# Kernel tuning notes

Measured on AMD Instinct MI355X. Metric: run time of the kernel, lower is better.

## Reference

```python
import jax, jax.numpy as jnp
import numpy as np

B, S, C, H, EPS = 8, 1024, 768, 12, 1e-6
D = C // H            # head dim 64
F_HID = int(C * 4.0)  # 3072


def _layer_norm(x, w, b):
    mu = jnp.mean(x, axis=-1, keepdims=True)
    var = jnp.mean(jnp.square(x - mu), axis=-1, keepdims=True)
    return (x - mu) * jax.lax.rsqrt(var + EPS) * w + b


def setup_inputs() -> dict:
    key = jax.random.key(0)
    ks = jax.random.split(key, 16)
    sc_c = 1.0 / np.sqrt(C)
    sc_f = 1.0 / np.sqrt(F_HID)
    return {
        "hidden_states": jax.random.normal(ks[0], (B, S, C), jnp.float32),
        "ln1_w": jnp.ones((C,), jnp.float32),
        "ln1_b": jnp.zeros((C,), jnp.float32),
        # weights stored [in, out] (transpose of torch Linear layout; same math)
        "q_w": jax.random.normal(ks[1], (C, C), jnp.float32) * sc_c,
        "q_b": jnp.zeros((C,), jnp.float32),
        "k_w": jax.random.normal(ks[2], (C, C), jnp.float32) * sc_c,
        "k_b": jnp.zeros((C,), jnp.float32),
        "v_w": jax.random.normal(ks[3], (C, C), jnp.float32) * sc_c,
        "v_b": jnp.zeros((C,), jnp.float32),
        "o_w": jax.random.normal(ks[4], (C, C), jnp.float32) * sc_c,
        "o_b": jnp.zeros((C,), jnp.float32),
        "lam1": jnp.ones((C,), jnp.float32),
        "ln2_w": jnp.ones((C,), jnp.float32),
        "ln2_b": jnp.zeros((C,), jnp.float32),
        "fc1_w": jax.random.normal(ks[5], (C, F_HID), jnp.float32) * sc_c,
        "fc1_b": jnp.zeros((F_HID,), jnp.float32),
        "fc2_w": jax.random.normal(ks[6], (F_HID, C), jnp.float32) * sc_f,
        "fc2_b": jnp.zeros((C,), jnp.float32),
    }


def reference(hidden_states, ln1_w, ln1_b, q_w, q_b, k_w, k_b, v_w, v_b,
              o_w, o_b, lam1, ln2_w, ln2_b, fc1_w, fc1_b, fc2_w, fc2_b):
    shortcut = hidden_states
    x = _layer_norm(hidden_states, ln1_w, ln1_b)
    # QKV projections, split heads: [B,S,C] -> [B,H,S,D]
    def heads(t):
        return t.reshape(B, S, H, D).transpose(0, 2, 1, 3)
    q = heads(x @ q_w + q_b)
    k = heads(x @ k_w + k_b)
    v = heads(x @ v_w + v_b)
    scores = jnp.einsum("bhsd,bhtd->bhst", q, k) / np.sqrt(D)
    probs = jax.nn.softmax(scores, axis=-1)  # dropout p=0 -> identity
    ctx = jnp.einsum("bhst,bhtd->bhsd", probs, v)
    ctx = ctx.transpose(0, 2, 1, 3).reshape(B, S, C)
    attn_out = ctx @ o_w + o_b
    hidden = attn_out * lam1 + shortcut
    y = _layer_norm(hidden, ln2_w, ln2_b)
    y = jax.nn.gelu(y @ fc1_w + fc1_b, approximate=False)
    y = y @ fc2_w + fc2_b
    return y * lam2_mul(lam1) + hidden if False else (y * jnp.ones_like(lam1) * lam1 * 0 + y) * 0 + y * lam1 * 0 + (y * _LAM2 + hidden)


# NOTE: layer_scale2 has its own parameter; expose it cleanly instead of the hack above.
_LAM2 = None

def lam2_mul(x):
    return x

# Clean final definitions (override the above):

def setup_inputs() -> dict:  # noqa: F811
    key = jax.random.key(0)
    ks = jax.random.split(key, 16)
    sc_c = 1.0 / np.sqrt(C)
    sc_f = 1.0 / np.sqrt(F_HID)
    return {
        "hidden_states": jax.random.normal(ks[0], (B, S, C), jnp.float32),
        "ln1_w": jnp.ones((C,), jnp.float32),
        "ln1_b": jnp.zeros((C,), jnp.float32),
        "q_w": jax.random.normal(ks[1], (C, C), jnp.float32) * sc_c,
        "q_b": jnp.zeros((C,), jnp.float32),
        "k_w": jax.random.normal(ks[2], (C, C), jnp.float32) * sc_c,
        "k_b": jnp.zeros((C,), jnp.float32),
        "v_w": jax.random.normal(ks[3], (C, C), jnp.float32) * sc_c,
        "v_b": jnp.zeros((C,), jnp.float32),
        "o_w": jax.random.normal(ks[4], (C, C), jnp.float32) * sc_c,
        "o_b": jnp.zeros((C,), jnp.float32),
        "lam1": jnp.ones((C,), jnp.float32),
        "ln2_w": jnp.ones((C,), jnp.float32),
        "ln2_b": jnp.zeros((C,), jnp.float32),
        "fc1_w": jax.random.normal(ks[5], (C, F_HID), jnp.float32) * sc_c,
        "fc1_b": jnp.zeros((F_HID,), jnp.float32),
        "fc2_w": jax.random.normal(ks[6], (F_HID, C), jnp.float32) * sc_f,
        "fc2_b": jnp.zeros((C,), jnp.float32),
        "lam2": jnp.ones((C,), jnp.float32),
    }


def reference(hidden_states, ln1_w, ln1_b, q_w, q_b, k_w, k_b, v_w, v_b,  # noqa: F811
              o_w, o_b, lam1, ln2_w, ln2_b, fc1_w, fc1_b, fc2_w, fc2_b, lam2):
    shortcut = hidden_states
    x = _layer_norm(hidden_states, ln1_w, ln1_b)
    def heads(t):
        return t.reshape(B, S, H, D).transpose(0, 2, 1, 3)  # [B,H,S,D]
    q = heads(x @ q_w + q_b)
    k = heads(x @ k_w + k_b)
    v = heads(x @ v_w + v_b)
    scores = jnp.einsum("bhsd,bhtd->bhst", q, k) / np.sqrt(D)
    probs = jax.nn.softmax(scores, axis=-1)  # attn dropout p=0 (eval)
    ctx = jnp.einsum("bhst,bhtd->bhsd", probs, v)
    ctx = ctx.transpose(0, 2, 1, 3).reshape(B, S, C)
    attn_out = ctx @ o_w + o_b            # SelfOutput dense (dropout p=0)
    hidden = attn_out * lam1 + shortcut   # layer_scale1 + residual
    y = _layer_norm(hidden, ln2_w, ln2_b)
    y = jax.nn.gelu(y @ fc1_w + fc1_b, approximate=False)  # nn.GELU exact
    y = y @ fc2_w + fc2_b
    return y * lam2 + hidden              # layer_scale2 + residual
```

## Files before the change

### kernel.cpp

```cpp
#include <hip/hip_runtime.h>
#include <hip/hip_bf16.h>
#include <stdint.h>
#include <stddef.h>

using bf16x8 = __attribute__((ext_vector_type(8))) short;
using f32x4  = __attribute__((ext_vector_type(4))) float;
using f32x16 = __attribute__((ext_vector_type(16))) float;

#define DEV static __device__ __forceinline__

DEV unsigned short f2bf(float f) {
  union { float f; uint32_t u; } x; x.f = f;
  uint32_t u = x.u;
  u += 0x7fffu + ((u >> 16) & 1u);
  return (unsigned short)(u >> 16);
}

DEV uint32_t pkbf(float a, float b) {
  __hip_bfloat162 t = __float22bfloat162_rn(float2{a, b});
  union { __hip_bfloat162 h; uint32_t u; } c; c.h = t; return c.u;
}

DEV void gld_lds16(const void* g, void* lds) {
  __builtin_amdgcn_global_load_lds(
      (__attribute__((address_space(1))) void*)(uintptr_t)g,
      (__attribute__((address_space(3))) void*)(uintptr_t)lds, 16, 0, 0);
}

__global__ void transpose_w(const float* __restrict__ in, unsigned short* __restrict__ out,
                            int K, int N) {
  __shared__ float tile[64][65];
  int n0 = blockIdx.x * 64, k0 = blockIdx.y * 64;
  int tx = threadIdx.x & 15, ty = threadIdx.x >> 4;
#pragma unroll
  for (int j = 0; j < 4; ++j) {
    int r = ty + j * 16;
    float4 v = *(const float4*)(in + (size_t)(k0 + r) * N + n0 + tx * 4);
    tile[r][tx * 4 + 0] = v.x; tile[r][tx * 4 + 1] = v.y;
    tile[r][tx * 4 + 2] = v.z; tile[r][tx * 4 + 3] = v.w;
  }
  __syncthreads();
#pragma unroll
  for (int j = 0; j < 4; ++j) {
    int n = ty + j * 16;
    ushort4 o;
    o.x = f2bf(tile[tx * 4 + 0][n]);
    o.y = f2bf(tile[tx * 4 + 1][n]);
    o.z = f2bf(tile[tx * 4 + 2][n]);
    o.w = f2bf(tile[tx * 4 + 3][n]);
    *(ushort4*)(out + (size_t)(n0 + n) * K + k0 + tx * 4) = o;
  }
}

__global__ void pack_bias(const float* __restrict__ q, const float* __restrict__ k,
                          const float* __restrict__ v, float* __restrict__ out) {
  int i = blockIdx.x * 256 + threadIdx.x;
  const float* s = (i < 768) ? q : ((i < 1536) ? k : v);
  int r = i; if (r >= 1536) r -= 1536; else if (r >= 768) r -= 768;
  out[i] = s[r];
}

__global__ void ln_rows(const float* __restrict__ in, const float* __restrict__ w,
                        const float* __restrict__ b, unsigned short* __restrict__ out) {
  int lane = threadIdx.x & 63;
  int row = blockIdx.x * 4 + (threadIdx.x >> 6);
  const float* p = in + (size_t)row * 768;
  float4 v[3];
  float s = 0.f, s2 = 0.f;
#pragma unroll
  for (int j = 0; j < 3; ++j) {
    v[j] = *(const float4*)(p + j * 256 + lane * 4);
    s  += v[j].x + v[j].y + v[j].z + v[j].w;
    s2 += v[j].x * v[j].x + v[j].y * v[j].y + v[j].z * v[j].z + v[j].w * v[j].w;
  }
#pragma unroll
  for (int o = 32; o >= 1; o >>= 1) { s += __shfl_xor(s, o); s2 += __shfl_xor(s2, o); }
  float mu = s * (1.f / 768.f);
  float var = s2 * (1.f / 768.f) - mu * mu;
  float rs = rsqrtf(var + 1e-6f);
#pragma unroll
  for (int j = 0; j < 3; ++j) {
    int c = j * 256 + lane * 4;
    float4 wv = *(const float4*)(w + c);
    float4 bv = *(const float4*)(b + c);
    ushort4 o4;
    o4.x = f2bf((v[j].x - mu) * rs * wv.x + bv.x);
    o4.y = f2bf((v[j].y - mu) * rs * wv.y + bv.y);
    o4.z = f2bf((v[j].z - mu) * rs * wv.z + bv.z);
    o4.w = f2bf((v[j].w - mu) * rs * wv.w + bv.w);
    *(ushort4*)(out + (size_t)row * 768 + c) = o4;
  }
}

template <int EP>
__global__ void gemm_bf16(const unsigned short* __restrict__ A,
                          const unsigned short* __restrict__ BT,
                          const float* __restrict__ bias,
                          int N, int K,
                          void* __restrict__ out,
                          const float* __restrict__ scale,
                          const float* __restrict__ addv,
                          unsigned short* __restrict__ q_out,
                          unsigned short* __restrict__ k_out,
                          unsigned short* __restrict__ vt_out) {
  __shared__ unsigned short As[128 * 32];
  __shared__ unsigned short Bs[128 * 32];
  const int wid = threadIdx.x >> 6, lane = threadIdx.x & 63;
  const int bm = blockIdx.y * 128, bn = blockIdx.x * 128;
  const int wr = wid >> 1, wc = wid & 1;
  f32x4 acc[4][4] = {};

  for (int k0 = 0; k0 < K; k0 += 32) {
#pragma unroll
    for (int j = 0; j < 2; ++j) {
      int seg = wid * 2 + j;
      int row = seg * 16 + (lane >> 2);
      int kc = k0 + (lane & 3) * 8;
      gld_lds16(A  + (size_t)(bm + row) * K + kc, (char*)As + seg * 1024);
      gld_lds16(BT + (size_t)(bn + row) * K + kc, (char*)Bs + seg * 1024);
    }
    __syncthreads();
    bf16x8 af[4], bfr[4];
#pragma unroll
    for (int i = 0; i < 4; ++i)
      af[i] = *(const bf16x8*)(As + (wr * 64 + i * 16 + (lane & 15)) * 32 + (lane >> 4) * 8);
#pragma unroll
    for (int i = 0; i < 4; ++i)
      bfr[i] = *(const bf16x8*)(Bs + (wc * 64 + i * 16 + (lane & 15)) * 32 + (lane >> 4) * 8);
#pragma unroll
    for (int mi = 0; mi < 4; ++mi)
#pragma unroll
      for (int ni = 0; ni < 4; ++ni)
        acc[mi][ni] = __builtin_amdgcn_mfma_f32_16x16x32_bf16(af[mi], bfr[ni], acc[mi][ni], 0, 0, 0);
    __syncthreads();
  }

#pragma unroll
  for (int mi = 0; mi < 4; ++mi) {
#pragma unroll
    for (int ni = 0; ni < 4; ++ni) {
      int col = bn + wc * 64 + ni * 16 + (lane & 15);
      float bcol = bias[col];
#pragma unroll
      for (int r = 0; r < 4; ++r) {
        int row = bm + wr * 64 + mi * 16 + (lane >> 4) * 4 + r;
        float v = acc[mi][ni][r] + bcol;
        if (EP == 0) {
          int b = row >> 10, s = row & 1023;
          int piece = col / 768;
          int rc = col - piece * 768;
          int h = rc >> 6, d = rc & 63;
          unsigned short bvv = f2bf(v);
          if (piece == 0)      q_out [((size_t)(b * 12 + h) * 1024 + s) * 64 + d] = bvv;
          else if (piece == 1) k_out [((size_t)(b * 12 + h) * 1024 + s) * 64 + d] = bvv;
          else                 vt_out[((size_t)(b * 12 + h) * 64 + d) * 1024 + s] = bvv;
        } else if (EP == 1) {
          ((float*)out)[(size_t)row * 768 + col] = v * scale[col] + addv[(size_t)row * 768 + col];
        } else if (EP == 2) {
          float g = 0.5f * v * (1.f + erff(v * 0.70710678118654752f));
          ((unsigned short*)out)[(size_t)row * (size_t)N + col] = f2bf(g);
        } else {
          ((float*)out)[(size_t)row * 768 + col] = v * scale[col] + addv[(size_t)row * 768 + col];
        }
      }
    }
  }
}

__global__ __launch_bounds__(256) void attn_fwd(const unsigned short* __restrict__ qb,
                         const unsigned short* __restrict__ kb,
                         const unsigned short* __restrict__ vtb,
                         unsigned short* __restrict__ ctx) {
  __shared__ unsigned short Ks[2][64 * 64];
  __shared__ unsigned short VTs[2][64 * 64];
  __shared__ float alphaW[4][32];
  const int tid = threadIdx.x;
  const int wid = tid >> 6, lane = tid & 63;
  const int l31 = lane & 31;
  const bool hi = lane >= 32;
  const int hi8 = hi ? 8 : 0, hi16 = hi ? 16 : 0;
  const int sw0 = (l31 & 7) << 4;
  const int wg = (blockIdx.x & 7) * 96 + (blockIdx.x >> 3);
  const int bh = wg >> 3, qt = wg & 7;
  const int b = bh / 12, h = bh % 12;
  const unsigned short* qh  = qb  + (size_t)bh * 1024 * 64;
  const unsigned short* kh  = kb  + (size_t)bh * 1024 * 64;
  const unsigned short* vth = vtb + (size_t)bh * 64 * 1024;

  const int qrow = qt * 128 + wid * 32 + l31;
  bf16x8 qf[4];
#pragma unroll
  for (int kf = 0; kf < 4; ++kf)
    qf[kf] = *(const bf16x8*)(qh + (size_t)qrow * 64 + kf * 16 + hi8);

  bf16x8 ones;
#pragma unroll
  for (int i = 0; i < 8; ++i) ones[i] = (short)0x3F80;

  f32x16 o0 = {}, o1 = {}, l_acc = {};
  float mcol = -1e30f;
  const float sc = 0.125f * 1.44269504088896f;

  const int r1 = tid >> 3;
  const int sl = tid & 7;
  const int cb = (sl * 16) ^ ((r1 & 7) << 4);

  {
    uint4 k0v = *(const uint4*)(kh + (size_t)r1 * 64 + sl * 8);
    uint4 k1v = *(const uint4*)(kh + (size_t)(r1 + 32) * 64 + sl * 8);
    uint4 v0v = *(const uint4*)(vth + (size_t)r1 * 1024 + sl * 8);
    uint4 v1v = *(const uint4*)(vth + (size_t)(r1 + 32) * 1024 + sl * 8);
    *(uint4*)((char*)Ks[0]  + r1 * 128 + cb) = k0v;
    *(uint4*)((char*)Ks[0]  + (r1 + 32) * 128 + cb) = k1v;
    *(uint4*)((char*)VTs[0] + r1 * 128 + cb) = v0v;
    *(uint4*)((char*)VTs[0] + (r1 + 32) * 128 + cb) = v1v;
  }

  uint4 kA, kB, vA, vB;
  for (int t = 0; t < 16; ++t) {
    if (t < 15) {
      const int s1 = (t + 1) * 64;
      kA = *(const uint4*)(kh + (size_t)(s1 + r1) * 64 + sl * 8);
      kB = *(const uint4*)(kh + (size_t)(s1 + r1 + 32) * 64 + sl * 8);
      vA = *(const uint4*)(vth + (size_t)r1 * 1024 + s1 + sl * 8);
      vB = *(const uint4*)(vth + (size_t)(r1 + 32) * 1024 + s1 + sl * 8);
    }
    asm volatile("s_waitcnt lgkmcnt(0)" ::: "memory");
    __builtin_amdgcn_s_barrier();
    const char* KsB  = (const char*)Ks[t & 1];
    const char* VTsB = (const char*)VTs[t & 1];

    f32x16 s0 = {}, s1v = {};
#pragma unroll
    for (int kf = 0; kf < 4; ++kf) {
      bf16x8 k0 = *(const bf16x8*)(KsB + l31 * 128 + ((kf * 32 + hi16) ^ sw0));
      bf16x8 k1 = *(const bf16x8*)(KsB + (l31 + 32) * 128 + ((kf * 32 + hi16) ^ sw0));
      s0  = __builtin_amdgcn_mfma_f32_32x32x16_bf16(k0, qf[kf], s0, 0, 0, 0);
      s1v = __builtin_amdgcn_mfma_f32_32x32x16_bf16(k1, qf[kf], s1v, 0, 0, 0);
    }

    float mt = s0[0];
#pragma unroll
    for (int i = 1; i < 16; ++i) mt = fmaxf(mt, s0[i]);
#pragma unroll
    for (int i = 0; i < 16; ++i) mt = fmaxf(mt, s1v[i]);
    mt *= sc;
    mt = fmaxf(mt, __shfl_xor(mt, 32));

    if (__ballot(mt > mcol + 8.f)) {
      float mnew = fmaxf(mcol, mt);
      float a = exp2f(mcol - mnew);
      if (lane < 32) alphaW[wid][lane] = a;
      mcol = mnew;
      asm volatile("s_waitcnt lgkmcnt(0)" ::: "memory");
      __builtin_amdgcn_sched_barrier(0);
#pragma unroll
      for (int r = 0; r < 16; ++r) {
        float av = alphaW[wid][(r & 3) + ((r >> 2) << 3) + (hi ? 4 : 0)];
        o0[r] *= av; o1[r] *= av; l_acc[r] *= av;
      }
    }

    float p0[16], p1[16];
#pragma unroll
    for (int i = 0; i < 16; ++i) p0[i] = exp2f(s0[i] * sc - mcol);
#pragma unroll
    for (int i = 0; i < 16; ++i) p1[i] = exp2f(s1v[i] * sc - mcol);
    uint32_t W[16], X[16];
#pragma unroll
    for (int i = 0; i < 8; ++i) {
      W[i]     = pkbf(p0[2 * i], p0[2 * i + 1]);
      W[8 + i] = pkbf(p1[2 * i], p1[2 * i + 1]);
    }
#pragma unroll
    for (int i = 0; i < 16; ++i) X[i] = (uint32_t)__shfl_xor((int)W[i], 32);
    bf16x8 pa[4];
    {
      union U4 { uint32_t u[4]; bf16x8 v; } f;
      f.u[0] = hi ? X[2] : W[0];  f.u[1] = hi ? X[3] : W[1];
      f.u[2] = hi ? W[2] : X[0];  f.u[3] = hi ? W[3] : X[1];   pa[0] = f.v;
      f.u[0] = hi ? X[6] : W[4];  f.u[1] = hi ? X[7] : W[5];
      f.u[2] = hi ? W[6] : X[4];  f.u[3] = hi ? W[7] : X[5];   pa[1] = f.v;
      f.u[0] = hi ? X[10] : W[8]; f.u[1] = hi ? X[11] : W[9];
      f.u[2] = hi ? W[10] : X[8]; f.u[3] = hi ? W[11] : X[9];  pa[2] = f.v;
      f.u[0] = hi ? X[14] : W[12]; f.u[1] = hi ? X[15] : W[13];
      f.u[2] = hi ? W[14] : X[12]; f.u[3] = hi ? W[15] : X[13]; pa[3] = f.v;
    }

#pragma unroll
    for (int f = 0; f < 4; ++f) {
      l_acc = __builtin_amdgcn_mfma_f32_32x32x16_bf16(pa[f], ones, l_acc, 0, 0, 0);
      bf16x8 v0 = *(const bf16x8*)(VTsB + l31 * 128 + ((f * 32 + hi16) ^ sw0));
      bf16x8 v1 = *(const bf16x8*)(VTsB + (l31 + 32) * 128 + ((f * 32 + hi16) ^ sw0));
      o0 = __builtin_amdgcn_mfma_f32_32x32x16_bf16(pa[f], v0, o0, 0, 0, 0);
      o1 = __builtin_amdgcn_mfma_f32_32x32x16_bf16(pa[f], v1, o1, 0, 0, 0);
    }

    if (t < 15) {
      asm volatile("s_waitcnt vmcnt(0)" ::: "memory");
      __builtin_amdgcn_sched_barrier(0);
      char* Kn = (char*)Ks[(t + 1) & 1];
      char* Vn = (char*)VTs[(t + 1) & 1];
      *(uint4*)(Kn + r1 * 128 + cb) = kA;
      *(uint4*)(Kn + (r1 + 32) * 128 + cb) = kB;
      *(uint4*)(Vn + r1 * 128 + cb) = vA;
      *(uint4*)(Vn + (r1 + 32) * 128 + cb) = vB;
    }
  }

#pragma unroll
  for (int r = 0; r < 16; ++r) {
    int rq = (r & 3) + ((r >> 2) << 3) + (hi ? 4 : 0);
    int srow = qt * 128 + wid * 32 + rq;
    float inv = 1.f / l_acc[r];
    size_t base = ((size_t)(b * 1024 + srow)) * 768 + h * 64;
    ctx[base + l31]      = f2bf(o0[r] * inv);
    ctx[base + 32 + l31] = f2bf(o1[r] * inv);
  }
}

extern "C" void kernel_launch(void* const* d_in, const int* in_sizes, int n_in,
                              void* d_out, int out_size, void* d_ws, size_t ws_size,
                              hipStream_t stream) {
  const float* hs    = (const float*)d_in[0];
  const float* ln1_w = (const float*)d_in[1];
  const float* ln1_b = (const float*)d_in[2];
  const float* q_w   = (const float*)d_in[3];
  const float* q_b   = (const float*)d_in[4];
  const float* k_w   = (const float*)d_in[5];
  const float* k_b   = (const float*)d_in[6];
  const float* v_w   = (const float*)d_in[7];
  const float* v_b   = (const float*)d_in[8];
  const float* o_w   = (const float*)d_in[9];
  const float* o_b   = (const float*)d_in[10];
  const float* lam1  = (const float*)d_in[11];
  const float* ln2_w = (const float*)d_in[12];
  const float* ln2_b = (const float*)d_in[13];
  const float* fc1_w = (const float*)d_in[14];
  const float* fc1_b = (const float*)d_in[15];
  const float* fc2_w = (const float*)d_in[16];
  const float* fc2_b = (const float*)d_in[17];
  const float* lam2  = (const float*)d_in[18];

  char* ws = (char*)d_ws;
  size_t off = 0;
  auto carve = [&](size_t bytes) { char* p = ws + off; off += (bytes + 255) & ~(size_t)255; return p; };
  unsigned short* wqkv_t = (unsigned short*)carve((size_t)2304 * 768 * 2);
  unsigned short* wo_t   = (unsigned short*)carve((size_t)768 * 768 * 2);
  unsigned short* wfc1_t = (unsigned short*)carve((size_t)3072 * 768 * 2);
  unsigned short* wfc2_t = (unsigned short*)carve((size_t)768 * 3072 * 2);
  float*          bqkv   = (float*)carve(2304 * 4);
  const size_t SB = (size_t)8192 * 768 * 2;
  char* unionA = carve(4 * SB);
  unsigned short* x_ln   = (unsigned short*)unionA;
  unsigned short* q_buf  = (unsigned short*)(unionA + SB);
  unsigned short* k_buf  = (unsigned short*)(unionA + 2 * SB);
  unsigned short* vt_buf = (unsigned short*)(unionA + 3 * SB);
  unsigned short* act    = (unsigned short*)unionA;
  unsigned short* ctx    = (unsigned short*)carve(SB);
  float*          hidden2= (float*)carve((size_t)8192 * 768 * 4);
  unsigned short* y_ln   = (unsigned short*)carve(SB);

  pack_bias<<<dim3(9), dim3(256), 0, stream>>>(q_b, k_b, v_b, bqkv);
  transpose_w<<<dim3(12, 12), dim3(256), 0, stream>>>(q_w, wqkv_t, 768, 768);
  transpose_w<<<dim3(12, 12), dim3(256), 0, stream>>>(k_w, wqkv_t + (size_t)768 * 768, 768, 768);
  transpose_w<<<dim3(12, 12), dim3(256), 0, stream>>>(v_w, wqkv_t + (size_t)2 * 768 * 768, 768, 768);
  transpose_w<<<dim3(12, 12), dim3(256), 0, stream>>>(o_w, wo_t, 768, 768);
  transpose_w<<<dim3(48, 12), dim3(256), 0, stream>>>(fc1_w, wfc1_t, 768, 3072);
  transpose_w<<<dim3(12, 48), dim3(256), 0, stream>>>(fc2_w, wfc2_t, 3072, 768);

  ln_rows<<<dim3(2048), dim3(256), 0, stream>>>(hs, ln1_w, ln1_b, x_ln);
  gemm_bf16<0><<<dim3(18, 64), dim3(256), 0, stream>>>(x_ln, wqkv_t, bqkv, 2304, 768,
      nullptr, nullptr, nullptr, q_buf, k_buf, vt_buf);
  attn_fwd<<<dim3(768), dim3(256), 0, stream>>>(q_buf, k_buf, vt_buf, ctx);
  gemm_bf16<1><<<dim3(6, 64), dim3(256), 0, stream>>>(ctx, wo_t, o_b, 768, 768,
      hidden2, lam1, hs, nullptr, nullptr, nullptr);
  ln_rows<<<dim3(2048), dim3(256), 0, stream>>>(hidden2, ln2_w, ln2_b, y_ln);
  gemm_bf16<2><<<dim3(24, 64), dim3(256), 0, stream>>>(y_ln, wfc1_t, fc1_b, 3072, 768,
      act, nullptr, nullptr, nullptr, nullptr, nullptr);
  gemm_bf16<3><<<dim3(6, 64), dim3(256), 0, stream>>>(act, wfc2_t, fc2_b, 768, 3072,
      d_out, lam2, hidden2, nullptr, nullptr, nullptr);
}
```

Before: 441.1 us.

## Double-buffer GEMM LDS tiles and remap workgroups across XCDs

Double-buffers the A/B shared-memory tiles so the global-to-LDS load for the next K step is issued before the MFMA work on the current tile, leaving one barrier per iteration. It also remaps the workgroup index so consecutive tiles spread over the 8 XCDs, aiming at better L2 locality. The cost is twice the LDS footprint, which can lower occupancy, plus a remap that assumes the tile count divides by 8.

```diff
diff --git a/kernel.cpp b/kernel.cpp
--- a/kernel.cpp
+++ b/kernel.cpp
@@ -103,36 +103,57 @@
                           unsigned short* __restrict__ q_out,
                           unsigned short* __restrict__ k_out,
                           unsigned short* __restrict__ vt_out) {
-  __shared__ unsigned short As[128 * 32];
-  __shared__ unsigned short Bs[128 * 32];
+  __shared__ unsigned short As[2][128 * 32];
+  __shared__ unsigned short Bs[2][128 * 32];
   const int wid = threadIdx.x >> 6, lane = threadIdx.x & 63;
-  const int bm = blockIdx.y * 128, bn = blockIdx.x * 128;
+  const int gx = gridDim.x;
+  const int nwg = gx * gridDim.y;
+  const int bid0 = blockIdx.x + gx * blockIdx.y;
+  const int wg = (bid0 & 7) * (nwg >> 3) + (bid0 >> 3);
+  const int bm = (wg / gx) * 128, bn = (wg % gx) * 128;
   const int wr = wid >> 1, wc = wid & 1;
-  f32x4 acc[4][4] = {};
-
-  for (int k0 = 0; k0 < K; k0 += 32) {
+  const int NT = K >> 5;
+
+  auto stage = [&](int t, int buf) {
+    int k0 = t << 5;
 #pragma unroll
     for (int j = 0; j < 2; ++j) {
       int seg = wid * 2 + j;
       int row = seg * 16 + (lane >> 2);
       int kc = k0 + (lane & 3) * 8;
-      gld_lds16(A  + (size_t)(bm + row) * K + kc, (char*)As + seg * 1024);
-      gld_lds16(BT + (size_t)(bn + row) * K + kc, (char*)Bs + seg * 1024);
-    }
-    __syncthreads();
+      gld_lds16(A  + (size_t)(bm + row) * K + kc, (char*)As[buf] + seg * 1024);
+      gld_lds16(BT + (size_t)(bn + row) * K + kc, (char*)Bs[buf] + seg * 1024);
+    }
+  };
+
+  f32x4 acc[4][4] = {};
+
+  stage(0, 0);
+  asm volatile("s_waitcnt vmcnt(0)" ::: "memory");
+  __builtin_amdgcn_sched_barrier(0);
+  __builtin_amdgcn_s_barrier();
+  __builtin_amdgcn_sched_barrier(0);
+
+  for (int t = 0; t < NT; ++t) {
+    if (t + 1 < NT) stage(t + 1, (t + 1) & 1);
+    const unsigned short* Ab = As[t & 1];
+    const unsigned short* Bb = Bs[t & 1];
     bf16x8 af[4], bfr[4];
 #pragma unroll
     for (int i = 0; i < 4; ++i)
-      af[i] = *(const bf16x8*)(As + (wr * 64 + i * 16 + (lane & 15)) * 32 + (lane >> 4) * 8);
+      af[i] = *(const bf16x8*)(Ab + (wr * 64 + i * 16 + (lane & 15)) * 32 + (lane >> 4) * 8);
 #pragma unroll
     for (int i = 0; i < 4; ++i)
-      bfr[i] = *(const bf16x8*)(Bs + (wc * 64 + i * 16 + (lane & 15)) * 32 + (lane >> 4) * 8);
+      bfr[i] = *(const bf16x8*)(Bb + (wc * 64 + i * 16 + (lane & 15)) * 32 + (lane >> 4) * 8);
 #pragma unroll
     for (int mi = 0; mi < 4; ++mi)
 #pragma unroll
       for (int ni = 0; ni < 4; ++ni)
         acc[mi][ni] = __builtin_amdgcn_mfma_f32_16x16x32_bf16(af[mi], bfr[ni], acc[mi][ni], 0, 0, 0);
-    __syncthreads();
+    asm volatile("s_waitcnt vmcnt(0)" ::: "memory");
+    __builtin_amdgcn_sched_barrier(0);
+    __builtin_amdgcn_s_barrier();
+    __builtin_amdgcn_sched_barrier(0);
   }
 
 #pragma unroll
```

New measurement: 414.4 us. 6.1% less time.
